# Performance work log

Measured on AMD Instinct MI355X. Metric: run time of the kernel, lower is better.

## Reference

```python
import jax, jax.numpy as jnp
import numpy as np

EPS = 1e-5  # 'eps' forward arg, fixed as in typical transformer LayerNorm


def setup_inputs() -> dict:
    key = jax.random.key(0)
    ks = jax.random.split(key, 9)
    B, S, D = 4, 2048, 2048
    scale = 0.02
    return {
        "inputs": jax.random.normal(ks[0], (B, S, D), jnp.float32),
        "norm_weight": jax.random.uniform(ks[1], (D,), jnp.float32),
        "norm_bias": jax.random.normal(ks[2], (D,), jnp.float32) * scale,
        "q_weight": jax.random.normal(ks[3], (D, D), jnp.float32) * scale,
        "q_bias": jax.random.normal(ks[4], (D,), jnp.float32) * scale,
        "k_weight": jax.random.normal(ks[5], (D, D), jnp.float32) * scale,
        "k_bias": jax.random.normal(ks[6], (D,), jnp.float32) * scale,
        "v_weight": jax.random.normal(ks[7], (D, D), jnp.float32) * scale,
        "v_bias": jax.random.normal(ks[8], (D,), jnp.float32) * scale,
        "trans_b": 1,
        "shape_param": 0,
    }


def _layernorm(x, w, b, eps):
    mu = jnp.mean(x, axis=-1, keepdims=True)
    var = jnp.mean(jnp.square(x - mu), axis=-1, keepdims=True)
    return (x - mu) * jax.lax.rsqrt(var + eps) * w + b


def reference(inputs, norm_weight, norm_bias, q_weight, q_bias,
              k_weight, k_bias, v_weight, v_bias, trans_b, shape_param):
    # fused LayerNorm + Q/K/V projection (torch_mlu_ops.fused_norm_attention_project)
    normed = _layernorm(inputs, norm_weight, norm_bias, EPS)
    # trans_b==True convention: weights are [out, in] (nn.Linear layout)
    if not trans_b:
        q_weight = q_weight.T
        k_weight = None if k_weight is None else k_weight.T
        v_weight = None if v_weight is None else v_weight.T
    q = jnp.einsum('bsd,od->bso', normed, q_weight) + q_bias
    outs = [q]
    if k_weight is not None:
        outs.append(jnp.einsum('bsd,od->bso', normed, k_weight) + k_bias)
    if v_weight is not None:
        outs.append(jnp.einsum('bsd,od->bso', normed, v_weight) + v_bias)
    output = jnp.concatenate(outs, axis=-1)  # [B, S, 3*D] fused QKV
    if shape_param:
        output = output.reshape(shape_param)
    return output
```

## Files before the change

### kernel.cpp

```cpp
#include <hip/hip_runtime.h>
#include <hip/hip_bf16.h>
#include <stdint.h>

__device__ __forceinline__ uint16_t f2bf(float f) {
    union { float f; uint32_t u; } c; c.f = f;
    uint32_t u = c.u;
    return (uint16_t)((u + 0x7FFFu + ((u >> 16) & 1u)) >> 16);
}
__device__ __forceinline__ uint32_t pack2(float a, float b) {
    return (uint32_t)f2bf(a) | ((uint32_t)f2bf(b) << 16);
}

typedef __bf16 bf16x8 __attribute__((ext_vector_type(8)));
typedef float  f32x4  __attribute__((ext_vector_type(4)));

#define GLOAD_LDS16(g, l) __builtin_amdgcn_global_load_lds( \
    (const __attribute__((address_space(1))) void*)(g),     \
    (__attribute__((address_space(3))) void*)(l), 16, 0, 0)

#define FENCE() asm volatile("" ::: "memory")

__global__ __launch_bounds__(256) void ln_kernel(
    const float* __restrict__ x, const float* __restrict__ gw,
    const float* __restrict__ gb, uint16_t* __restrict__ y, int D)
{
    const int t = threadIdx.x;
    const size_t row = blockIdx.x;
    const float4* xr = (const float4*)(x + row * (size_t)D);
    float4 v0 = xr[2 * t], v1 = xr[2 * t + 1];

    float s  = v0.x + v0.y + v0.z + v0.w + v1.x + v1.y + v1.z + v1.w;
    float ss = v0.x * v0.x + v0.y * v0.y + v0.z * v0.z + v0.w * v0.w
             + v1.x * v1.x + v1.y * v1.y + v1.z * v1.z + v1.w * v1.w;
#pragma unroll
    for (int off = 32; off > 0; off >>= 1) {
        s  += __shfl_down(s, off);
        ss += __shfl_down(ss, off);
    }
    __shared__ float red[10];
    const int wave = t >> 6, lane = t & 63;
    if (lane == 0) { red[wave] = s; red[4 + wave] = ss; }
    __syncthreads();
    if (t == 0) {
        float S  = red[0] + red[1] + red[2] + red[3];
        float SS = red[4] + red[5] + red[6] + red[7];
        float mu = S / (float)D;
        float var = SS / (float)D - mu * mu;
        red[8] = mu;
        red[9] = rsqrtf(var + 1e-5f);
    }
    __syncthreads();
    const float mu = red[8], rstd = red[9];

    const float4* wr = (const float4*)gw;
    const float4* br = (const float4*)gb;
    float4 w0 = wr[2 * t], w1 = wr[2 * t + 1];
    float4 b0 = br[2 * t], b1 = br[2 * t + 1];

    uint4 ov;
    ov.x = pack2((v0.x - mu) * rstd * w0.x + b0.x, (v0.y - mu) * rstd * w0.y + b0.y);
    ov.y = pack2((v0.z - mu) * rstd * w0.z + b0.z, (v0.w - mu) * rstd * w0.w + b0.w);
    ov.z = pack2((v1.x - mu) * rstd * w1.x + b1.x, (v1.y - mu) * rstd * w1.y + b1.y);
    ov.w = pack2((v1.z - mu) * rstd * w1.z + b1.z, (v1.w - mu) * rstd * w1.w + b1.w);
    ((uint4*)(y + row * (size_t)D))[t] = ov;
}

__global__ __launch_bounds__(256) void wcvt_kernel(
    const float* __restrict__ wq, const float* __restrict__ wk,
    const float* __restrict__ wv, uint16_t* __restrict__ out)
{
    const size_t i = ((size_t)blockIdx.x * 256 + threadIdx.x) * 8;
    const int which = (int)(i >> 22);
    const float* src = (which == 0) ? wq : (which == 1) ? wk : wv;
    const size_t off = i & ((1u << 22) - 1);
    float4 a = *(const float4*)(src + off);
    float4 b = *(const float4*)(src + off + 4);
    uint4 ov;
    ov.x = pack2(a.x, a.y);
    ov.y = pack2(a.z, a.w);
    ov.z = pack2(b.x, b.y);
    ov.w = pack2(b.z, b.w);
    *(uint4*)(out + i) = ov;
}


#define STAGE_A(H, KT, SL) do {                                               \
    const uint16_t* g_ = gA + (size_t)((H) * 128) * K + (KT) * 64;            \
    char* l_ = (char*)lds + (((SL) * 2 + (H)) * 16384) + t * 16;              \
    GLOAD_LDS16(g_, l_);                                                      \
    GLOAD_LDS16(g_ + (size_t)64 * K, l_ + 8192);                              \
} while (0)

#define STAGE_B(H, KT, SL) do {                                               \
    const uint16_t* g_ = gB + (size_t)((H) * 128) * K + (KT) * 64;            \
    char* l_ = (char*)lds + 65536 + (((SL) * 2 + (H)) * 16384) + t * 16;      \
    GLOAD_LDS16(g_, l_);                                                      \
    GLOAD_LDS16(g_ + (size_t)64 * K, l_ + 8192);                              \
} while (0)

#define PHASE(P, ABASE, STAGE_CODE, PREBAR, TAILWAIT)                         \
  {                                                                           \
    bf16x8 Af[2][2];                                                          \
    _Pragma("unroll") for (int m_ = 0; m_ < 2; ++m_)                          \
      _Pragma("unroll") for (int s_ = 0; s_ < 2; ++s_)                        \
        Af[m_][s_] = *(const bf16x8*)((const char*)lds + (ABASE) + aoff       \
                                      + (2 * (P) + m_) * 2048 + s_ * 64);     \
    STAGE_CODE                                                                \
    PREBAR                                                                    \
    __builtin_amdgcn_s_barrier();                                             \
    asm volatile("s_waitcnt lgkmcnt(0)" ::: "memory");                        \
    __builtin_amdgcn_s_setprio(1);                                            \
    _Pragma("unroll") for (int s_ = 0; s_ < 2; ++s_)                          \
      _Pragma("unroll") for (int m_ = 0; m_ < 2; ++m_)                        \
        _Pragma("unroll") for (int j_ = 0; j_ < 4; ++j_)                      \
          acc[2 * (P) + m_][j_] = __builtin_amdgcn_mfma_f32_16x16x32_bf16(    \
              Af[m_][s_], Bf[j_][s_], acc[2 * (P) + m_][j_], 0, 0, 0);        \
    __builtin_amdgcn_s_setprio(0);                                            \
    TAILWAIT                                                                  \
    __builtin_amdgcn_s_barrier();                                             \
    FENCE();                                                                  \
  }

#define KTILE(SLOT, KT, SA, SB, TAILWAIT)                                     \
  {                                                                           \
    const int ab_ = ((SLOT) * 2 + wr) * 16384;                                \
    const int bb_ = 65536 + ((SLOT) * 2 + (wc >> 1)) * 16384;                 \
    bf16x8 Bf[4][2];                                                          \
    _Pragma("unroll") for (int j_ = 0; j_ < 4; ++j_)                          \
      _Pragma("unroll") for (int s_ = 0; s_ < 2; ++s_)                        \
        Bf[j_][s_] = *(const bf16x8*)((const char*)lds + bb_ + boff           \
                                      + j_ * 2048 + s_ * 64);                 \
    PHASE(0, ab_, { if (SA) STAGE_A(0, (KT) + 1, (SLOT) ^ 1); },              \
          asm volatile("s_waitcnt lgkmcnt(8)" ::: "memory");, )               \
    PHASE(1, ab_, { if (SA) STAGE_A(1, (KT) + 1, (SLOT) ^ 1); }, , )          \
    PHASE(2, ab_, { if (SB) STAGE_B(0, (KT) + 2, (SLOT)); }, , )              \
    PHASE(3, ab_, { if (SB) STAGE_B(1, (KT) + 2, (SLOT)); }, , TAILWAIT)      \
  }

__global__ __launch_bounds__(512, 2) void qkv_gemm256(
    const uint16_t* __restrict__ A, const uint16_t* __restrict__ W,
    const float* __restrict__ Bq, const float* __restrict__ Bk,
    const float* __restrict__ Bv, float* __restrict__ C,
    int M, int N, int K)
{
    (void)M;
    extern __shared__ uint16_t lds[];
    const int t = threadIdx.x;
    const int lane = t & 63, wid = t >> 6;
    const int wr = wid >> 2, wc = wid & 3;
    const int fr = lane & 15;
    const int fq2 = (lane >> 4) * 16;

    const int nbt = N >> 8;
    const int nwg = gridDim.x;
    int bid = blockIdx.x;
    int swz = (nwg & 7) ? bid : ((bid & 7) * (nwg >> 3) + (bid >> 3));
    const int mb = swz / nbt, nb = swz % nbt;

    const int sx = (fr & 4) ? 32 : 0;
    const int koff = fq2 ^ sx;
    const int aoff = fr * 128 + koff;
    const int boff = ((wc & 1) * 64 + fr) * 128 + koff;

    const int srow = t >> 3;
    const int scol = ((t & 7) * 8) ^ (((t >> 5) & 1) << 4);
    const uint16_t* gA = A + (size_t)(mb * 256 + srow) * K + scol;
    const uint16_t* gB = W + (size_t)(nb * 256 + srow) * K + scol;

    f32x4 acc[8][4] = {};
    const int NT = K >> 6;

    STAGE_B(0, 0, 0); STAGE_B(1, 0, 0);
    STAGE_A(0, 0, 0); STAGE_A(1, 0, 0);
    STAGE_B(0, 1, 1); STAGE_B(1, 1, 1);
    asm volatile("s_waitcnt vmcnt(4)" ::: "memory");
    __builtin_amdgcn_s_barrier();
    FENCE();

#pragma unroll 1
    for (int i = 0; i < (NT >> 1) - 1; ++i) {
        const int k0 = i << 1;
        KTILE(0, k0,     1, 1, asm volatile("s_waitcnt vmcnt(4)" ::: "memory");)
        KTILE(1, k0 + 1, 1, 1, asm volatile("s_waitcnt vmcnt(4)" ::: "memory");)
    }
    KTILE(0, NT - 2, 1, 0, asm volatile("s_waitcnt vmcnt(0)" ::: "memory");)
    KTILE(1, NT - 1, 0, 0, )

    const int r0 = mb * 256 + wr * 128 + (lane >> 4) * 4;
    const int c0 = nb * 256 + wc * 64 + fr;
    const float* bp = (nb < 8) ? Bq : (nb < 16) ? Bk : Bv;
    const int cb = (nb & 7) * 256 + wc * 64 + fr;
    float bj[4];
#pragma unroll
    for (int j = 0; j < 4; ++j) bj[j] = bp[cb + j * 16];
#pragma unroll
    for (int i = 0; i < 8; ++i)
#pragma unroll
        for (int j = 0; j < 4; ++j)
#pragma unroll
            for (int r = 0; r < 4; ++r)
                C[(size_t)(r0 + i * 16 + r) * N + c0 + j * 16] = acc[i][j][r] + bj[j];
}

extern "C" void kernel_launch(void* const* d_in, const int* in_sizes, int n_in,
                              void* d_out, int out_size, void* d_ws, size_t ws_size,
                              hipStream_t stream) {
    const float* x  = (const float*)d_in[0];
    const float* nw = (const float*)d_in[1];
    const float* nb = (const float*)d_in[2];
    const float* wq = (const float*)d_in[3];
    const float* bq = (const float*)d_in[4];
    const float* wk = (const float*)d_in[5];
    const float* bk = (const float*)d_in[6];
    const float* wv = (const float*)d_in[7];
    const float* bv = (const float*)d_in[8];

    const int D = in_sizes[1];
    const int M = in_sizes[0] / D;
    const int N = 3 * D;

    static bool attr_done = false;
    if (!attr_done) {
        hipFuncSetAttribute((const void*)qkv_gemm256,
                            hipFuncAttributeMaxDynamicSharedMemorySize, 131072);
        attr_done = true;
    }

    uint16_t* normed = (uint16_t*)d_ws;
    uint16_t* wcat   = normed + (size_t)M * D;

    ln_kernel<<<M, 256, 0, stream>>>(x, nw, nb, normed, D);
    wcvt_kernel<<<((size_t)N * D) / (256 * 8), 256, 0, stream>>>(wq, wk, wv, wcat);
    const int grid = (M / 256) * (N / 256);
    qkv_gemm256<<<grid, 512, 131072, stream>>>(normed, wcat, bq, bk, bv,
                                               (float*)d_out, M, N, D);
}
```

Measured before the change: 472.3 us.

## Use full XOR LDS swizzle and banded XCD-aware tile mapping in QKV GEMM

Replaces the partial LDS swizzle (one bit keyed on row bit 2) with a full 3-bit XOR swizzle of the 16-byte k-chunk by row index. The global-to-LDS staging columns and the fragment read offsets are changed to match. The goal is to remove LDS bank conflicts on the bf16x8 fragment reads. It also remaps workgroups so each XCD covers a contiguous band of M tiles with groups of 8 N tiles, aiming for better L2 reuse of A and W. The mapping relies on the grid shape meeting divisibility conditions, and the staging and read swizzles must stay consistent or results will be wrong.

Result: no change. 464.2 us (-1.7%).

```diff
diff --git a/kernel.cpp b/kernel.cpp
--- a/kernel.cpp
+++ b/kernel.cpp
@@ -103,8 +103,9 @@
     bf16x8 Af[2][2];                                                          \
     _Pragma("unroll") for (int m_ = 0; m_ < 2; ++m_)                          \
       _Pragma("unroll") for (int s_ = 0; s_ < 2; ++s_)                        \
-        Af[m_][s_] = *(const bf16x8*)((const char*)lds + (ABASE) + aoff       \
-                                      + (2 * (P) + m_) * 2048 + s_ * 64);     \
+        Af[m_][s_] = *(const bf16x8*)((const char*)lds + (ABASE)              \
+                                      + (aoff ^ (s_ << 6))                    \
+                                      + (2 * (P) + m_) * 2048);               \
     STAGE_CODE                                                                \
     PREBAR                                                                    \
     __builtin_amdgcn_s_barrier();                                             \
@@ -128,8 +129,8 @@
     bf16x8 Bf[4][2];                                                          \
     _Pragma("unroll") for (int j_ = 0; j_ < 4; ++j_)                          \
       _Pragma("unroll") for (int s_ = 0; s_ < 2; ++s_)                        \
-        Bf[j_][s_] = *(const bf16x8*)((const char*)lds + bb_ + boff           \
-                                      + j_ * 2048 + s_ * 64);                 \
+        Bf[j_][s_] = *(const bf16x8*)((const char*)lds + bb_                  \
+                                      + (boff ^ (s_ << 6)) + j_ * 2048);      \
     PHASE(0, ab_, { if (SA) STAGE_A(0, (KT) + 1, (SLOT) ^ 1); },              \
           asm volatile("s_waitcnt lgkmcnt(8)" ::: "memory");, )               \
     PHASE(1, ab_, { if (SA) STAGE_A(1, (KT) + 1, (SLOT) ^ 1); }, , )          \
@@ -153,17 +154,28 @@
 
     const int nbt = N >> 8;
     const int nwg = gridDim.x;
-    int bid = blockIdx.x;
-    int swz = (nwg & 7) ? bid : ((bid & 7) * (nwg >> 3) + (bid >> 3));
-    const int mb = swz / nbt, nb = swz % nbt;
-
-    const int sx = (fr & 4) ? 32 : 0;
-    const int koff = fq2 ^ sx;
-    const int aoff = fr * 128 + koff;
-    const int boff = ((wc & 1) * 64 + fr) * 128 + koff;
+    int mb, nb;
+    if ((nwg & 7) == 0) {
+        const int cpx = nwg >> 3;
+        const int xcd = blockIdx.x & 7, ti = blockIdx.x >> 3;
+        if (cpx % nbt == 0 && (nbt & 7) == 0) {
+            const int band = ti >> 5, r = ti & 31;
+            mb = xcd * (cpx / nbt) + (r >> 3);
+            nb = (band << 3) + (r & 7);
+        } else {
+            const int swz = xcd * cpx + ti;
+            mb = swz / nbt; nb = swz % nbt;
+        }
+    } else {
+        mb = blockIdx.x / nbt; nb = blockIdx.x % nbt;
+    }
+
+    const int kbase = fq2 ^ ((fr & 7) << 4);
+    const int aoff = fr * 128 + kbase;
+    const int boff = ((wc & 1) * 64 + fr) * 128 + kbase;
 
     const int srow = t >> 3;
-    const int scol = ((t & 7) * 8) ^ (((t >> 5) & 1) << 4);
+    const int scol = (((t & 7) ^ ((t >> 3) & 7)) << 3);
     const uint16_t* gA = A + (size_t)(mb * 256 + srow) * K + scol;
     const uint16_t* gB = W + (size_t)(nb * 256 + srow) * K + scol;
 
```
